# Kernel optimization log

Measured on AMD Instinct MI355X. Metric: run time of the kernel, lower is better.

Reference implementation:

```python
import jax, jax.numpy as jnp
import numpy as np

T, H, N = 4096, 2048, 1024  # seq_length, d_model, d_hidden
MAX_PHASE = 6.28


def setup_inputs() -> dict:
    key = jax.random.key(0)
    ks = jax.random.split(key, 9)
    inputs = jax.random.normal(ks[0], (T, H), dtype=jnp.float32)
    # LRU init (exp_param=True, r_min=0, r_max=1): lambda = exp(-exp(nu) + i*exp(theta))
    u1 = jax.random.uniform(ks[1], (N,), dtype=jnp.float32)
    u2 = jax.random.uniform(ks[2], (N,), dtype=jnp.float32)
    nu = jnp.log(-0.5 * jnp.log(u1))            # log-parameterized decay
    theta = jnp.log(MAX_PHASE * u2)             # log-parameterized phase
    # gamma_log = log(sqrt(1 - |lambda|^2)), |lambda| = exp(-exp(nu))
    gamma_log = 0.5 * jnp.log(1.0 - jnp.exp(-2.0 * jnp.exp(nu)) + 1e-8)
    B_re = jax.random.normal(ks[3], (N, H), dtype=jnp.float32) / np.sqrt(2 * H)
    B_im = jax.random.normal(ks[4], (N, H), dtype=jnp.float32) / np.sqrt(2 * H)
    C_re = jax.random.normal(ks[5], (H, N), dtype=jnp.float32) / np.sqrt(N)
    C_im = jax.random.normal(ks[6], (H, N), dtype=jnp.float32) / np.sqrt(N)
    D = jax.random.normal(ks[7], (H,), dtype=jnp.float32)
    return {"inputs": inputs, "nu": nu, "theta": theta, "gamma_log": gamma_log,
            "B_re": B_re, "B_im": B_im, "C_re": C_re, "C_im": C_im, "D": D}


def _binary_operator_diag(q_i, q_j):
    A_i, b_i = q_i
    A_j, b_j = q_j
    return (A_j * A_i, A_j * b_i + b_j)


def reference(inputs, nu, theta, gamma_log, B_re, B_im, C_re, C_im, D):
    # diag_lambda = exp(-exp(nu) + i*exp(theta))   (exp_param=True)
    diag_lambda = jnp.exp(-jnp.exp(nu) + 1j * jnp.exp(theta))      # [N] complex64
    gamma = jnp.exp(gamma_log)                                      # [N]
    B_norm = (B_re + 1j * B_im) * gamma[:, None]                    # [N, H] complex
    # Bu_t = B_norm @ u_t  ->  [T, N]
    Bu = inputs.astype(jnp.complex64) @ B_norm.T
    Lam = jnp.broadcast_to(diag_lambda[None, :], Bu.shape)          # [T, N]
    # parallel scan of diagonal linear recurrence h_t = lambda * h_{t-1} + Bu_t
    _, h = jax.lax.associative_scan(_binary_operator_diag, (Lam, Bu))
    C = C_re + 1j * C_im                                            # [H, N]
    # y_t = Re(C @ h_t) + D * u_t
    y = (h @ C.T).real + D[None, :] * inputs                        # [T, H]
    return y
```

## Files before the change

### kernel.cpp

```cpp
#include <hip/hip_runtime.h>
#include <math.h>

#define T_DIM 4096
#define H_DIM 2048
#define N_DIM 1024
#define N2    2048
#define KK    2048
#define CHUNK 64
#define NCHUNK (T_DIM / CHUNK)
#define NT    (KK / 64)

using u16    = unsigned short;
using u16x4  = __attribute__((ext_vector_type(4))) u16;
using bf16x8 = __attribute__((ext_vector_type(8))) short;
using f32x4  = __attribute__((ext_vector_type(4))) float;

typedef const __attribute__((address_space(1))) u16 glob_u16;
typedef __attribute__((address_space(3))) u16 lds_u16;

__device__ inline void gload16(const u16* g, u16* l) {
    __builtin_amdgcn_global_load_lds((glob_u16*)g, (lds_u16*)l, 16, 0, 0);
}

__device__ inline u16 f2bf(float x) {
    unsigned u = __builtin_bit_cast(unsigned, x);
    u += 0x7fffu + ((u >> 16) & 1u);
    return (u16)(u >> 16);
}
__device__ inline float bf2f(u16 x) {
    return __builtin_bit_cast(float, (unsigned)x << 16);
}

__global__ __launch_bounds__(256) void cvt_u_k(const float* __restrict__ X,
                                               u16* __restrict__ Y) {
    size_t i = ((size_t)blockIdx.x * 256 + threadIdx.x) * 4;
    float4 v = *(const float4*)(X + i);
    u16x4 o = { f2bf(v.x), f2bf(v.y), f2bf(v.z), f2bf(v.w) };
    *(u16x4*)(Y + i) = o;
}

__global__ __launch_bounds__(256) void cvt_b_k(const float* __restrict__ Bre,
                                               const float* __restrict__ Bim,
                                               const float* __restrict__ glog,
                                               u16* __restrict__ Bcat) {
    size_t i = ((size_t)blockIdx.x * 256 + threadIdx.x) * 4;
    int n = (int)(i >> 11);
    size_t h = i & 2047;
    int nn = n & (N_DIM - 1);
    float g = expf(glog[nn]);
    const float* src = (n < N_DIM ? Bre : Bim) + (size_t)nn * H_DIM + h;
    float4 v = *(const float4*)src;
    u16x4 o = { f2bf(v.x * g), f2bf(v.y * g), f2bf(v.z * g), f2bf(v.w * g) };
    *(u16x4*)(Bcat + i) = o;
}

__global__ __launch_bounds__(256) void cvt_c_k(const float* __restrict__ Cre,
                                               const float* __restrict__ Cim,
                                               u16* __restrict__ Ccat) {
    size_t i = ((size_t)blockIdx.x * 256 + threadIdx.x) * 4;
    int hrow = (int)(i >> 11);
    int n = (int)(i & 2047);
    float sgn = 1.f;
    const float* src;
    if (n < N_DIM) src = Cre + (size_t)hrow * N_DIM + n;
    else { src = Cim + (size_t)hrow * N_DIM + (n - N_DIM); sgn = -1.f; }
    float4 v = *(const float4*)src;
    u16x4 o = { f2bf(v.x * sgn), f2bf(v.y * sgn), f2bf(v.z * sgn), f2bf(v.w * sgn) };
    *(u16x4*)(Ccat + i) = o;
}

template <int EPI>
__global__ __launch_bounds__(256, 2) void gemm_pipe(
    const u16* __restrict__ A, const u16* __restrict__ B,
    void* __restrict__ Cout, const float* __restrict__ D,
    const u16* __restrict__ Ubf)
{
    __shared__ u16 lds[40960];

    const int tid  = threadIdx.x;
    const int wave = tid >> 6, lane = tid & 63;
    const int nbid = (blockIdx.x & 7) * 64 + (blockIdx.x >> 3);
    const int bm = nbid >> 4;
    const int bn = nbid & 15;
    const size_t row0 = (size_t)bm * 128;
    const size_t col0 = (size_t)bn * 128;
    const int wr = wave >> 1, wc = wave & 1;
    const int fr = lane & 15, fq = lane >> 4;

    const int srow = tid >> 3;
    const int skc  = (tid & 7) ^ (srow & 7);
    const u16* aSrc = A + (row0 + srow) * KK + skc * 8;
    const u16* bSrc = B + (col0 + srow) * KK + skc * 8;

    const int aOff = (wr * 64 + fr) * 64;
    const int bOff = (wc * 64 + fr) * 64;
    const int swz0 = ((fq)     ^ (fr & 7)) * 8;
    const int swz1 = ((4 + fq) ^ (fr & 7)) * 8;

    f32x4 acc[4][4] = {};

    auto STAGE_A = [&](int buf, int kt) {
#pragma unroll
        for (int u = 0; u < 4; ++u)
            gload16(aSrc + (size_t)u * 32 * KK + kt * 64,
                    &lds[buf * 8192 + u * 2048 + wave * 512]);
    };
    auto STAGE_B = [&](int buf, int kt) {
#pragma unroll
        for (int u = 0; u < 4; ++u)
            gload16(bSrc + (size_t)u * 32 * KK + kt * 64,
                    &lds[24576 + buf * 8192 + u * 2048 + wave * 512]);
    };

    bf16x8 fa[4], fb[4], ga[4], gb[4];

    auto READ_F = [&](const u16* Ab, const u16* Bb, int swz) {
#pragma unroll
        for (int m = 0; m < 4; ++m) fa[m] = *(const bf16x8*)&Ab[aOff + m * 1024 + swz];
#pragma unroll
        for (int n = 0; n < 4; ++n) fb[n] = *(const bf16x8*)&Bb[bOff + n * 1024 + swz];
    };
    auto READ_G = [&](const u16* Ab, const u16* Bb, int swz) {
#pragma unroll
        for (int m = 0; m < 4; ++m) ga[m] = *(const bf16x8*)&Ab[aOff + m * 1024 + swz];
#pragma unroll
        for (int n = 0; n < 4; ++n) gb[n] = *(const bf16x8*)&Bb[bOff + n * 1024 + swz];
    };
    auto MFMA_F = [&]() {
        __builtin_amdgcn_s_setprio(1);
#pragma unroll
        for (int m = 0; m < 4; ++m)
#pragma unroll
            for (int n = 0; n < 4; ++n)
                acc[m][n] = __builtin_amdgcn_mfma_f32_16x16x32_bf16(
                    fa[m], fb[n], acc[m][n], 0, 0, 0);
        __builtin_amdgcn_s_setprio(0);
    };
    auto MFMA_G = [&]() {
        __builtin_amdgcn_s_setprio(1);
#pragma unroll
        for (int m = 0; m < 4; ++m)
#pragma unroll
            for (int n = 0; n < 4; ++n)
                acc[m][n] = __builtin_amdgcn_mfma_f32_16x16x32_bf16(
                    ga[m], gb[n], acc[m][n], 0, 0, 0);
        __builtin_amdgcn_s_setprio(0);
    };

    STAGE_A(0, 0); STAGE_B(0, 0); STAGE_A(1, 1);
    asm volatile("s_waitcnt vmcnt(4)" ::: "memory");
    __builtin_amdgcn_s_barrier();
    READ_F(&lds[0], &lds[24576], swz0);

    int a_cur = 0;
    for (int t = 0; t < NT; ++t) {
        const u16* Ab = &lds[a_cur * 8192];
        const u16* Bb = &lds[24576 + (t & 1) * 8192];

        if (t + 1 < NT) STAGE_B((t + 1) & 1, t + 1);
        MFMA_F();
        if (t + 2 < NT) {
            int a_nxt = a_cur + 2; if (a_nxt >= 3) a_nxt -= 3;
            STAGE_A(a_nxt, t + 2);
        }
        READ_G(Ab, Bb, swz1);
        MFMA_G();

        if (t + 1 < NT) {
            if (t + 2 < NT) asm volatile("s_waitcnt vmcnt(4)" ::: "memory");
            else            asm volatile("s_waitcnt vmcnt(0)" ::: "memory");
            __builtin_amdgcn_s_barrier();
            int a_n = a_cur + 1; if (a_n == 3) a_n = 0;
            READ_F(&lds[a_n * 8192], &lds[24576 + ((t + 1) & 1) * 8192], swz0);
        }
        ++a_cur; if (a_cur == 3) a_cur = 0;
    }

    const int crow = (int)row0 + wr * 64 + fq * 4;
    const int ccol = (int)col0 + wc * 64 + fr;
    float dc[4];
    if constexpr (EPI) {
#pragma unroll
        for (int n = 0; n < 4; ++n) dc[n] = D[ccol + n * 16];
    }
#pragma unroll
    for (int m = 0; m < 4; ++m)
#pragma unroll
        for (int n = 0; n < 4; ++n) {
            int cc = ccol + n * 16;
#pragma unroll
            for (int j = 0; j < 4; ++j) {
                int r = crow + m * 16 + j;
                size_t p = (size_t)r * N2 + cc;
                float v = acc[m][n][j];
                if constexpr (EPI)
                    ((float*)Cout)[p] = v + dc[n] * bf2f(Ubf[p]);
                else
                    ((u16*)Cout)[p] = f2bf(v);
            }
        }
}

__global__ __launch_bounds__(256) void carry_pass_k(const u16* __restrict__ Bu,
                                                    const float* __restrict__ nu,
                                                    const float* __restrict__ theta,
                                                    float* __restrict__ car) {
    int idx = blockIdx.x * 256 + threadIdx.x;
    int chan = idx & (N_DIM - 1);
    int chunk = idx >> 10;
    float a = expf(nu[chan]), b = expf(theta[chan]);
    float m = expf(-a), s, c;
    __sincosf(b, &s, &c);
    float lr = m * c, li = m * s;
    float hr = 0.f, hi = 0.f;
    size_t base = (size_t)chunk * CHUNK * N2 + chan;
    for (int i = 0; i < CHUNK; ++i) {
        size_t p = base + (size_t)i * N2;
        float br = bf2f(Bu[p]), bi = bf2f(Bu[p + N_DIM]);
        float nr = fmaf(lr, hr, fmaf(-li, hi, br));
        float ni = fmaf(lr, hi, fmaf(li, hr, bi));
        hr = nr; hi = ni;
    }
    car[(size_t)chunk * N2 + chan] = hr;
    car[(size_t)chunk * N2 + N_DIM + chan] = hi;
}

__global__ __launch_bounds__(256) void scan_carry_k(float* __restrict__ car,
                                                    const float* __restrict__ nu,
                                                    const float* __restrict__ theta) {
    __shared__ float sR[NCHUNK][65], sI[NCHUNK][65];
    int tid = threadIdx.x;
    int chan0 = blockIdx.x * 64;
    for (int i = tid; i < NCHUNK * 64; i += 256) {
        int ck = i >> 6, c = i & 63;
        sR[ck][c] = car[(size_t)ck * N2 + chan0 + c];
        sI[ck][c] = car[(size_t)ck * N2 + N_DIM + chan0 + c];
    }
    __syncthreads();
    if (tid < 64) {
        int chan = chan0 + tid;
        float a = expf(nu[chan]), b = expf(theta[chan]);
        float m = expf(-(float)CHUNK * a), s, c;
        __sincosf((float)CHUNK * b, &s, &c);
        float lr = m * c, li = m * s;
        float hr = sR[0][tid], hi = sI[0][tid];
        for (int ck = 1; ck < NCHUNK; ++ck) {
            float nr = fmaf(lr, hr, fmaf(-li, hi, sR[ck][tid]));
            float ni = fmaf(lr, hi, fmaf(li, hr, sI[ck][tid]));
            hr = nr; hi = ni;
            sR[ck][tid] = hr; sI[ck][tid] = hi;
        }
    }
    __syncthreads();
    for (int i = tid; i < NCHUNK * 64; i += 256) {
        int ck = i >> 6, c = i & 63;
        car[(size_t)ck * N2 + chan0 + c] = sR[ck][c];
        car[(size_t)ck * N2 + N_DIM + chan0 + c] = sI[ck][c];
    }
}

__global__ __launch_bounds__(256) void scan_out_k(const u16* __restrict__ Bu,
                                                  const float* __restrict__ car,
                                                  const float* __restrict__ nu,
                                                  const float* __restrict__ theta,
                                                  u16* __restrict__ Hbf) {
    int idx = blockIdx.x * 256 + threadIdx.x;
    int chan = idx & (N_DIM - 1);
    int chunk = idx >> 10;
    float a = expf(nu[chan]), b = expf(theta[chan]);
    float m = expf(-a), s, c;
    __sincosf(b, &s, &c);
    float lr = m * c, li = m * s;
    float hr = 0.f, hi = 0.f;
    if (chunk > 0) {
        size_t cp = (size_t)(chunk - 1) * N2 + chan;
        hr = car[cp]; hi = car[cp + N_DIM];
    }
    size_t base = (size_t)chunk * CHUNK * N2 + chan;
    for (int i = 0; i < CHUNK; ++i) {
        size_t p = base + (size_t)i * N2;
        float br = bf2f(Bu[p]), bi = bf2f(Bu[p + N_DIM]);
        float nr = fmaf(lr, hr, fmaf(-li, hi, br));
        float ni = fmaf(lr, hi, fmaf(li, hr, bi));
        hr = nr; hi = ni;
        Hbf[p] = f2bf(hr);
        Hbf[p + N_DIM] = f2bf(hi);
    }
}

extern "C" void kernel_launch(void* const* d_in, const int* in_sizes, int n_in,
                              void* d_out, int out_size, void* d_ws, size_t ws_size,
                              hipStream_t stream) {
    const float* U     = (const float*)d_in[0];
    const float* nu    = (const float*)d_in[1];
    const float* theta = (const float*)d_in[2];
    const float* glog  = (const float*)d_in[3];
    const float* Bre   = (const float*)d_in[4];
    const float* Bim   = (const float*)d_in[5];
    const float* Cre   = (const float*)d_in[6];
    const float* Cim   = (const float*)d_in[7];
    const float* Dp    = (const float*)d_in[8];
    float* Y = (float*)d_out;

    u16* Ubf  = (u16*)d_ws;
    u16* Bcat = Ubf + (size_t)T_DIM * H_DIM;
    u16* Ccat = Bcat + (size_t)N2 * H_DIM;
    u16* Hbf  = Ccat + (size_t)H_DIM * N2;
    u16* Bu   = Hbf + (size_t)T_DIM * N2;
    float* car = (float*)(Bu + (size_t)T_DIM * N2);

    cvt_u_k<<<(T_DIM * H_DIM / 4) / 256, 256, 0, stream>>>(U, Ubf);
    cvt_b_k<<<((size_t)N2 * H_DIM / 4) / 256, 256, 0, stream>>>(Bre, Bim, glog, Bcat);
    cvt_c_k<<<((size_t)H_DIM * N2 / 4) / 256, 256, 0, stream>>>(Cre, Cim, Ccat);

    gemm_pipe<0><<<512, 256, 0, stream>>>(Ubf, Bcat, (void*)Bu, nullptr, nullptr);

    carry_pass_k<<<(NCHUNK * N_DIM) / 256, 256, 0, stream>>>(Bu, nu, theta, car);
    scan_carry_k<<<N_DIM / 64, 256, 0, stream>>>(car, nu, theta);
    scan_out_k<<<(NCHUNK * N_DIM) / 256, 256, 0, stream>>>(Bu, car, nu, theta, Hbf);

    gemm_pipe<1><<<512, 256, 0, stream>>>(Hbf, Ccat, (void*)Y, Dp, Ubf);
}
```

Baseline: 114.1 us.

## Split GEMM K-halves across 8 waves with LDS reduction; fuse conversion kernels

The GEMM block grows from 256 to 512 threads. Each pair of waves now splits the two 32-wide k-halves of every 64-wide tile instead of one wave doing both, and the partial accumulators are reduced through LDS before the epilogue. Staging is redistributed so each wave issues fewer global-to-LDS loads per tile. The three fp32-to-bf16 conversion kernels are merged into one launch to save launch overhead. The aim is more waves per CU to hide latency, at the cost of an extra LDS reduction pass and barriers. The __launch_bounds__(512,4) request may also squeeze registers.

```diff
diff --git a/kernel.cpp b/kernel.cpp
--- a/kernel.cpp
+++ b/kernel.cpp
@@ -31,46 +31,44 @@
     return __builtin_bit_cast(float, (unsigned)x << 16);
 }
 
-__global__ __launch_bounds__(256) void cvt_u_k(const float* __restrict__ X,
-                                               u16* __restrict__ Y) {
-    size_t i = ((size_t)blockIdx.x * 256 + threadIdx.x) * 4;
-    float4 v = *(const float4*)(X + i);
-    u16x4 o = { f2bf(v.x), f2bf(v.y), f2bf(v.z), f2bf(v.w) };
-    *(u16x4*)(Y + i) = o;
-}
-
-__global__ __launch_bounds__(256) void cvt_b_k(const float* __restrict__ Bre,
-                                               const float* __restrict__ Bim,
-                                               const float* __restrict__ glog,
-                                               u16* __restrict__ Bcat) {
-    size_t i = ((size_t)blockIdx.x * 256 + threadIdx.x) * 4;
-    int n = (int)(i >> 11);
-    size_t h = i & 2047;
-    int nn = n & (N_DIM - 1);
-    float g = expf(glog[nn]);
-    const float* src = (n < N_DIM ? Bre : Bim) + (size_t)nn * H_DIM + h;
-    float4 v = *(const float4*)src;
-    u16x4 o = { f2bf(v.x * g), f2bf(v.y * g), f2bf(v.z * g), f2bf(v.w * g) };
-    *(u16x4*)(Bcat + i) = o;
-}
-
-__global__ __launch_bounds__(256) void cvt_c_k(const float* __restrict__ Cre,
-                                               const float* __restrict__ Cim,
-                                               u16* __restrict__ Ccat) {
-    size_t i = ((size_t)blockIdx.x * 256 + threadIdx.x) * 4;
-    int hrow = (int)(i >> 11);
-    int n = (int)(i & 2047);
-    float sgn = 1.f;
-    const float* src;
-    if (n < N_DIM) src = Cre + (size_t)hrow * N_DIM + n;
-    else { src = Cim + (size_t)hrow * N_DIM + (n - N_DIM); sgn = -1.f; }
-    float4 v = *(const float4*)src;
-    u16x4 o = { f2bf(v.x * sgn), f2bf(v.y * sgn), f2bf(v.z * sgn), f2bf(v.w * sgn) };
-    *(u16x4*)(Ccat + i) = o;
+__global__ __launch_bounds__(256) void cvt_all_k(
+    const float* __restrict__ U, const float* __restrict__ Bre,
+    const float* __restrict__ Bim, const float* __restrict__ glog,
+    const float* __restrict__ Cre, const float* __restrict__ Cim,
+    u16* __restrict__ Ubf, u16* __restrict__ Bcat, u16* __restrict__ Ccat)
+{
+    int bid = blockIdx.x;
+    if (bid < 8192) {
+        size_t i = ((size_t)bid * 256 + threadIdx.x) * 4;
+        float4 v = *(const float4*)(U + i);
+        u16x4 o = { f2bf(v.x), f2bf(v.y), f2bf(v.z), f2bf(v.w) };
+        *(u16x4*)(Ubf + i) = o;
+    } else if (bid < 12288) {
+        size_t i = ((size_t)(bid - 8192) * 256 + threadIdx.x) * 4;
+        int n = (int)(i >> 11);
+        size_t h = i & 2047;
+        int nn = n & (N_DIM - 1);
+        float g = expf(glog[nn]);
+        const float* src = (n < N_DIM ? Bre : Bim) + (size_t)nn * H_DIM + h;
+        float4 v = *(const float4*)src;
+        u16x4 o = { f2bf(v.x * g), f2bf(v.y * g), f2bf(v.z * g), f2bf(v.w * g) };
+        *(u16x4*)(Bcat + i) = o;
+    } else {
+        size_t i = ((size_t)(bid - 12288) * 256 + threadIdx.x) * 4;
+        int hrow = (int)(i >> 11);
+        int n = (int)(i & 2047);
+        float sgn = 1.f;
+        const float* src;
+        if (n < N_DIM) src = Cre + (size_t)hrow * N_DIM + n;
+        else { src = Cim + (size_t)hrow * N_DIM + (n - N_DIM); sgn = -1.f; }
+        float4 v = *(const float4*)src;
+        u16x4 o = { f2bf(v.x * sgn), f2bf(v.y * sgn), f2bf(v.z * sgn), f2bf(v.w * sgn) };
+        *(u16x4*)(Ccat + i) = o;
+    }
 }
 
 template <int EPI>
-__global__ __launch_bounds__(256, 2) void gemm_pipe(
+__global__ __launch_bounds__(512, 4) void gemm_pipe(
     const u16* __restrict__ A, const u16* __restrict__ B,
     void* __restrict__ Cout, const float* __restrict__ D,
     const u16* __restrict__ Ubf)
@@ -84,49 +82,48 @@
     const int bn = nbid & 15;
     const size_t row0 = (size_t)bm * 128;
     const size_t col0 = (size_t)bn * 128;
-    const int wr = wave >> 1, wc = wave & 1;
+    const int kg = wave & 1;
+    const int wc = (wave >> 1) & 1;
+    const int wr = wave >> 2;
     const int fr = lane & 15, fq = lane >> 4;
 
-    const int srow = tid >> 3;
-    const int skc  = (tid & 7) ^ (srow & 7);
+    const int srow = wave * 16 + (lane >> 3);
+    const int skc  = (lane & 7) ^ ((lane >> 3) & 7);
     const u16* aSrc = A + (row0 + srow) * KK + skc * 8;
     const u16* bSrc = B + (col0 + srow) * KK + skc * 8;
-
-    const int aOff = (wr * 64 + fr) * 64;
-    const int bOff = (wc * 64 + fr) * 64;
-    const int swz0 = ((fq)     ^ (fr & 7)) * 8;
-    const int swz1 = ((4 + fq) ^ (fr & 7)) * 8;
+    const int stOff = wave * 1024;
+
+    const int slot8 = ((kg * 4 + fq) ^ (fr & 7)) * 8;
+    const int aOff = (wr * 64 + fr) * 64 + slot8;
+    const int bOff = (wc * 64 + fr) * 64 + slot8;
 
     f32x4 acc[4][4] = {};
 
     auto STAGE_A = [&](int buf, int kt) {
-#pragma unroll
-        for (int u = 0; u < 4; ++u)
-            gload16(aSrc + (size_t)u * 32 * KK + kt * 64,
-                    &lds[buf * 8192 + u * 2048 + wave * 512]);
+        gload16(aSrc + kt * 64,            &lds[buf * 8192 + stOff]);
+        gload16(aSrc + 8 * KK + kt * 64,   &lds[buf * 8192 + stOff + 512]);
     };
     auto STAGE_B = [&](int buf, int kt) {
-#pragma unroll
-        for (int u = 0; u < 4; ++u)
-            gload16(bSrc + (size_t)u * 32 * KK + kt * 64,
-                    &lds[24576 + buf * 8192 + u * 2048 + wave * 512]);
+        gload16(bSrc + kt * 64,            &lds[24576 + buf * 8192 + stOff]);
+        gload16(bSrc + 8 * KK + kt * 64,   &lds[24576 + buf * 8192 + stOff + 512]);
     };
 
-    bf16x8 fa[4], fb[4], ga[4], gb[4];
-
-    auto READ_F = [&](const u16* Ab, const u16* Bb, int swz) {
-#pragma unroll
-        for (int m = 0; m < 4; ++m) fa[m] = *(const bf16x8*)&Ab[aOff + m * 1024 + swz];
-#pragma unroll
-        for (int n = 0; n < 4; ++n) fb[n] = *(const bf16x8*)&Bb[bOff + n * 1024 + swz];
+    bf16x8 fa[4], fb[4];
+    auto READ_F = [&](const u16* Ab, const u16* Bb) {
+#pragma unroll
+        for (int m = 0; m < 4; ++m) fa[m] = *(const bf16x8*)&Ab[aOff + m * 1024];
+#pragma unroll
+        for (int n = 0; n < 4; ++n) fb[n] = *(const bf16x8*)&Bb[bOff + n * 1024];
     };
-    auto READ_G = [&](const u16* Ab, const u16* Bb, int swz) {
-#pragma unroll
-        for (int m = 0; m < 4; ++m) ga[m] = *(const bf16x8*)&Ab[aOff + m * 1024 + swz];
-#pragma unroll
-        for (int n = 0; n < 4; ++n) gb[n] = *(const bf16x8*)&Bb[bOff + n * 1024 + swz];
-    };
-    auto MFMA_F = [&]() {
+
+    STAGE_A(0, 0); STAGE_B(0, 0); STAGE_A(1, 1);
+    asm volatile("s_waitcnt vmcnt(2)" ::: "memory");
+    __builtin_amdgcn_s_barrier();
+    READ_F(&lds[0], &lds[24576]);
+
+    int a_cur = 0;
+    for (int t = 0; t < NT; ++t) {
+        if (t + 1 < NT) STAGE_B((t + 1) & 1, t + 1);
         __builtin_amdgcn_s_setprio(1);
 #pragma unroll
         for (int m = 0; m < 4; ++m)
@@ -135,70 +132,60 @@
                 acc[m][n] = __builtin_amdgcn_mfma_f32_16x16x32_bf16(
                     fa[m], fb[n], acc[m][n], 0, 0, 0);
         __builtin_amdgcn_s_setprio(0);
-    };
-    auto MFMA_G = [&]() {
-        __builtin_amdgcn_s_setprio(1);
-#pragma unroll
-        for (int m = 0; m < 4; ++m)
-#pragma unroll
-            for (int n = 0; n < 4; ++n)
-                acc[m][n] = __builtin_amdgcn_mfma_f32_16x16x32_bf16(
-                    ga[m], gb[n], acc[m][n], 0, 0, 0);
-        __builtin_amdgcn_s_setprio(0);
-    };
-
-    STAGE_A(0, 0); STAGE_B(0, 0); STAGE_A(1, 1);
-    asm volatile("s_waitcnt vmcnt(4)" ::: "memory");
-    __builtin_amdgcn_s_barrier();
-    READ_F(&lds[0], &lds[24576], swz0);
-
-    int a_cur = 0;
-    for (int t = 0; t < NT; ++t) {
-        const u16* Ab = &lds[a_cur * 8192];
-        const u16* Bb = &lds[24576 + (t & 1) * 8192];
-
-        if (t + 1 < NT) STAGE_B((t + 1) & 1, t + 1);
-        MFMA_F();
         if (t + 2 < NT) {
             int a_nxt = a_cur + 2; if (a_nxt >= 3) a_nxt -= 3;
             STAGE_A(a_nxt, t + 2);
         }
-        READ_G(Ab, Bb, swz1);
-        MFMA_G();
-
         if (t + 1 < NT) {
-            if (t + 2 < NT) asm volatile("s_waitcnt vmcnt(4)" ::: "memory");
+            if (t + 2 < NT) asm volatile("s_waitcnt vmcnt(2)" ::: "memory");
             else            asm volatile("s_waitcnt vmcnt(0)" ::: "memory");
             __builtin_amdgcn_s_barrier();
             int a_n = a_cur + 1; if (a_n == 3) a_n = 0;
-            READ_F(&lds[a_n * 8192], &lds[24576 + ((t + 1) & 1) * 8192], swz0);
+            READ_F(&lds[a_n * 8192], &lds[24576 + ((t + 1) & 1) * 8192]);
         }
         ++a_cur; if (a_cur == 3) a_cur = 0;
     }
 
-    const int crow = (int)row0 + wr * 64 + fq * 4;
-    const int ccol = (int)col0 + wc * 64 + fr;
-    float dc[4];
-    if constexpr (EPI) {
-#pragma unroll
-        for (int n = 0; n < 4; ++n) dc[n] = D[ccol + n * 16];
-    }
-#pragma unroll
-    for (int m = 0; m < 4; ++m)
-#pragma unroll
-        for (int n = 0; n < 4; ++n) {
-            int cc = ccol + n * 16;
-#pragma unroll
-            for (int j = 0; j < 4; ++j) {
-                int r = crow + m * 16 + j;
-                size_t p = (size_t)r * N2 + cc;
-                float v = acc[m][n][j];
-                if constexpr (EPI)
-                    ((float*)Cout)[p] = v + dc[n] * bf2f(Ubf[p]);
-                else
-                    ((u16*)Cout)[p] = f2bf(v);
+    __builtin_amdgcn_s_barrier();
+    const int pair = wr * 2 + wc;
+    float* lf = (float*)lds;
+    if (kg == 1) {
+#pragma unroll
+        for (int i = 0; i < 16; ++i)
+            *(f32x4*)&lf[pair * 4096 + i * 256 + lane * 4] = acc[i >> 2][i & 3];
+    }
+    asm volatile("s_waitcnt lgkmcnt(0)" ::: "memory");
+    __builtin_amdgcn_s_barrier();
+    if (kg == 0) {
+#pragma unroll
+        for (int i = 0; i < 16; ++i) {
+            f32x4 o = *(const f32x4*)&lf[pair * 4096 + i * 256 + lane * 4];
+            acc[i >> 2][i & 3] += o;
+        }
+        const int crow = (int)row0 + wr * 64 + fq * 4;
+        const int ccol = (int)col0 + wc * 64 + fr;
+        float dc[4];
+        if constexpr (EPI) {
+#pragma unroll
+            for (int n = 0; n < 4; ++n) dc[n] = D[ccol + n * 16];
+        }
+#pragma unroll
+        for (int m = 0; m < 4; ++m)
+#pragma unroll
+            for (int n = 0; n < 4; ++n) {
+                int cc = ccol + n * 16;
+#pragma unroll
+                for (int j = 0; j < 4; ++j) {
+                    int r = crow + m * 16 + j;
+                    size_t p = (size_t)r * N2 + cc;
+                    float v = acc[m][n][j];
+                    if constexpr (EPI)
+                        ((float*)Cout)[p] = v + dc[n] * bf2f(Ubf[p]);
+                    else
+                        ((u16*)Cout)[p] = f2bf(v);
+                }
             }
-        }
+    }
 }
 
 __global__ __launch_bounds__(256) void carry_pass_k(const u16* __restrict__ Bu,
@@ -309,15 +296,14 @@
     u16* Bu   = Hbf + (size_t)T_DIM * N2;
     float* car = (float*)(Bu + (size_t)T_DIM * N2);
 
-    cvt_u_k<<<(T_DIM * H_DIM / 4) / 256, 256, 0, stream>>>(U, Ubf);
-    cvt_b_k<<<((size_t)N2 * H_DIM / 4) / 256, 256, 0, stream>>>(Bre, Bim, glog, Bcat);
-    cvt_c_k<<<((size_t)H_DIM * N2 / 4) / 256, 256, 0, stream>>>(Cre, Cim, Ccat);
-
-    gemm_pipe<0><<<512, 256, 0, stream>>>(Ubf, Bcat, (void*)Bu, nullptr, nullptr);
+    cvt_all_k<<<16384, 256, 0, stream>>>(U, Bre, Bim, glog, Cre, Cim,
+                                         Ubf, Bcat, Ccat);
+
+    gemm_pipe<0><<<512, 512, 0, stream>>>(Ubf, Bcat, (void*)Bu, nullptr, nullptr);
 
     carry_pass_k<<<(NCHUNK * N_DIM) / 256, 256, 0, stream>>>(Bu, nu, theta, car);
     scan_carry_k<<<N_DIM / 64, 256, 0, stream>>>(car, nu, theta);
     scan_out_k<<<(NCHUNK * N_DIM) / 256, 256, 0, stream>>>(Bu, car, nu, theta, Hbf);
 
-    gemm_pipe<1><<<512, 256, 0, stream>>>(Hbf, Ccat, (void*)Y, Dp, Ubf);
-}
+    gemm_pipe<1><<<512, 512, 0, stream>>>(Hbf, Ccat, (void*)Y, Dp, Ubf);
+}
```

Result: faster. 111.6 us (-2.3%).
